# Optimization experiments

Measured on AMD Instinct MI355X. Metric: run time of the kernel, lower is better.

Reference implementation:

```python
import jax, jax.numpy as jnp
import numpy as np
import math

EMBED_DIM = 1024
NUM_HEADS = 16
HEAD_DIM = EMBED_DIM // NUM_HEADS
B, S = 4, 2048


def setup_inputs() -> dict:
    key = jax.random.key(0)
    ks = jax.random.split(key, 9)
    scale = 1.0 / math.sqrt(EMBED_DIM)
    def lin(k):
        kw, kb = jax.random.split(k)
        W = jax.random.uniform(kw, (EMBED_DIM, EMBED_DIM), jnp.float32, -scale, scale)
        b = jax.random.uniform(kb, (EMBED_DIM,), jnp.float32, -scale, scale)
        return W, b
    Wq, bq = lin(ks[0]); Wk, bk = lin(ks[1]); Wv, bv = lin(ks[2]); Wo, bo = lin(ks[3])
    x = jax.random.normal(ks[4], (B, S, EMBED_DIM), jnp.float32)
    return {"x": x, "Wq": Wq, "bq": bq, "Wk": Wk, "bk": bk,
            "Wv": Wv, "bv": bv, "Wo": Wo, "bo": bo}


def reference(x, Wq, bq, Wk, bk, Wv, bv, Wo, bo):
    Bx, Sx, E = x.shape
    def proj(W, b):
        y = jnp.einsum('bse,oe->bso', x, W) + b
        return y.reshape(Bx, Sx, NUM_HEADS, HEAD_DIM).transpose(0, 2, 1, 3)  # [B,H,S,D]
    q = proj(Wq, bq)
    k = proj(Wk, bk)
    v = proj(Wv, bv)
    scores = jnp.einsum('bhsd,bhtd->bhst', q, k) / math.sqrt(HEAD_DIM)
    # causal mask (paged_cache is None, seq_len > 1)
    causal = jnp.tril(jnp.ones((Sx, Sx), dtype=bool))
    scores = jnp.where(causal[None, None], scores, -jnp.inf)
    attn = jax.nn.softmax(scores, axis=-1)
    out = jnp.einsum('bhst,bhtd->bhsd', attn, v)
    out = out.transpose(0, 2, 1, 3).reshape(Bx, Sx, E)
    return jnp.einsum('bse,oe->bso', out, Wo) + bo
```

## Files before the change

### kernel.cpp

```cpp
#include <hip/hip_runtime.h>
#include <hip/hip_bf16.h>
#include <stdint.h>

#define EDIM 1024
#define NH   16
#define HD   64
#define BB   4
#define SS   2048
#define MROWS (BB*SS)

typedef __bf16 bf16x8 __attribute__((ext_vector_type(8)));
typedef __bf16 bf16x4 __attribute__((ext_vector_type(4)));
typedef float  f32x4  __attribute__((ext_vector_type(4)));
typedef float  f32x16 __attribute__((ext_vector_type(16)));
typedef int    int2v  __attribute__((ext_vector_type(2)));

__device__ __forceinline__ void async16(const void* g, void* lds) {
    __builtin_amdgcn_global_load_lds((__attribute__((address_space(1))) void*)(g),
                                     (__attribute__((address_space(3))) void*)(lds),
                                     16, 0, 0);
}

__device__ __forceinline__ f32x4 mfma16(bf16x8 a, bf16x8 b, f32x4 c) {
    return __builtin_amdgcn_mfma_f32_16x16x32_bf16(a, b, c, 0, 0, 0);
}
__device__ __forceinline__ f32x16 mfma32(bf16x8 a, bf16x8 b, f32x16 c) {
    return __builtin_amdgcn_mfma_f32_32x32x16_bf16(a, b, c, 0, 0, 0);
}

__device__ __forceinline__ int pkbf16(float a, float b) {
    union { __bf16 h[2]; int i; } u;
    u.h[0] = (__bf16)a; u.h[1] = (__bf16)b;
    return u.i;
}

__global__ __launch_bounds__(256) void cvt_kernel(const float* __restrict__ s,
                                                  __bf16* __restrict__ d, int n) {
    int i = (blockIdx.x * 256 + threadIdx.x) * 4;
    if (i < n) {
        float4 v = *reinterpret_cast<const float4*>(s + i);
        bf16x4 o;
        o.x = (__bf16)v.x; o.y = (__bf16)v.y; o.z = (__bf16)v.z; o.w = (__bf16)v.w;
        *reinterpret_cast<bf16x4*>(d + i) = o;
    }
}

__global__ __launch_bounds__(256) void cvt4_kernel(const float* __restrict__ s0,
                                                   const float* __restrict__ s1,
                                                   const float* __restrict__ s2,
                                                   const float* __restrict__ s3,
                                                   __bf16* __restrict__ d) {
    int m = blockIdx.x >> 10;
    const float* s = (m == 0) ? s0 : (m == 1) ? s1 : (m == 2) ? s2 : s3;
    int i = ((blockIdx.x & 1023) * 256 + threadIdx.x) * 4;
    float4 v = *reinterpret_cast<const float4*>(s + i);
    bf16x4 o;
    o.x = (__bf16)v.x; o.y = (__bf16)v.y; o.z = (__bf16)v.z; o.w = (__bf16)v.w;
    *reinterpret_cast<bf16x4*>(d + (size_t)m * (EDIM * EDIM) + i) = o;
}

struct GemmCtx {
    const __bf16 *ap0, *ap1, *bp0, *bp1;
    int wb0, wb1;
};

__device__ __forceinline__ void g_stage(GemmCtx& c, char* As, char* Bs) {
    async16(c.ap0, As + c.wb0);
    async16(c.ap1, As + c.wb1);
    async16(c.bp0, Bs + c.wb0);
    async16(c.bp1, Bs + c.wb1);
    c.ap0 += 32; c.ap1 += 32; c.bp0 += 32; c.bp1 += 32;
}

__device__ __forceinline__ void g_compute(const char* As, const char* Bs,
                                          int wm, int wn, int lrow, int lslot,
                                          f32x4 acc[4][4]) {
    bf16x8 af[4], bfr[4];
    #pragma unroll
    for (int mf = 0; mf < 4; ++mf) {
        int row = wm + mf * 16 + lrow;
        af[mf] = *reinterpret_cast<const bf16x8*>(As + row * 64 + ((lslot ^ (row & 3)) << 4));
    }
    #pragma unroll
    for (int nf = 0; nf < 4; ++nf) {
        int row = wn + nf * 16 + lrow;
        bfr[nf] = *reinterpret_cast<const bf16x8*>(Bs + row * 64 + ((lslot ^ (row & 3)) << 4));
    }
    __builtin_amdgcn_s_setprio(1);
    #pragma unroll
    for (int mf = 0; mf < 4; ++mf)
        #pragma unroll
        for (int nf = 0; nf < 4; ++nf)
            acc[mf][nf] = mfma16(af[mf], bfr[nf], acc[mf][nf]);
    __builtin_amdgcn_s_setprio(0);
}

#define GEMM_DBUF_LOOP()                                                      \
    g_stage(ctx, As0, Bs0);                                                   \
    for (int kt = 0; kt < 32; kt += 2) {                                      \
        g_stage(ctx, As1, Bs1);                                               \
        asm volatile("s_waitcnt vmcnt(4)" ::: "memory");                      \
        __builtin_amdgcn_s_barrier();                                         \
        __builtin_amdgcn_sched_barrier(0);                                    \
        g_compute(As0, Bs0, wm, wn, lrow, lslot, acc);                        \
        __builtin_amdgcn_sched_barrier(0);                                    \
        __builtin_amdgcn_s_barrier();                                         \
        if (kt + 2 < 32) {                                                    \
            g_stage(ctx, As0, Bs0);                                           \
            asm volatile("s_waitcnt vmcnt(4)" ::: "memory");                  \
        } else {                                                              \
            asm volatile("s_waitcnt vmcnt(0)" ::: "memory");                  \
        }                                                                     \
        __builtin_amdgcn_s_barrier();                                         \
        __builtin_amdgcn_sched_barrier(0);                                    \
        g_compute(As1, Bs1, wm, wn, lrow, lslot, acc);                        \
        __builtin_amdgcn_sched_barrier(0);                                    \
        __builtin_amdgcn_s_barrier();                                         \
    }

#define GEMM_PREAMBLE(Aptr, Wptr)                                             \
    const int tid = threadIdx.x;                                              \
    const int w = tid >> 6, l = tid & 63;                                     \
    const int bm = blockIdx.x * 128, bn = blockIdx.y * 128;                   \
    const int wm = (w >> 1) * 64, wn = (w & 1) * 64;                          \
    f32x4 acc[4][4] = {};                                                     \
    const int lrow = l & 15;                                                  \
    const int lslot = l >> 4;                                                 \
    const int row0 = tid >> 2, cb0 = tid & 3;                                 \
    const int row1 = 64 + row0;                                               \
    GemmCtx ctx;                                                              \
    ctx.ap0 = (Aptr) + (size_t)(bm + row0) * EDIM + ((cb0 ^ (row0 & 3)) << 3);\
    ctx.ap1 = (Aptr) + (size_t)(bm + row1) * EDIM + ((cb0 ^ (row1 & 3)) << 3);\
    ctx.bp0 = (Wptr) + (size_t)(bn + row0) * EDIM + ((cb0 ^ (row0 & 3)) << 3);\
    ctx.bp1 = (Wptr) + (size_t)(bn + row1) * EDIM + ((cb0 ^ (row1 & 3)) << 3);\
    ctx.wb0 = (w * 64) * 16;                                                  \
    ctx.wb1 = (256 + w * 64) * 16;

__global__ __launch_bounds__(256) void gemm_qkv(const __bf16* __restrict__ A,
                                                const __bf16* __restrict__ W,
                                                const float* __restrict__ bq,
                                                const float* __restrict__ bk,
                                                const float* __restrict__ bv,
                                                __bf16* __restrict__ Qb,
                                                __bf16* __restrict__ Kb,
                                                __bf16* __restrict__ Vtb) {
    __shared__ char As0[128 * 64], Bs0[128 * 64];
    __shared__ char As1[128 * 64], Bs1[128 * 64];
    GEMM_PREAMBLE(A, W)
    GEMM_DBUF_LOOP()

    const int mat = bn >> 10;
    const float* bias = (mat == 0) ? bq : (mat == 1) ? bk : bv;
    __bf16* qk = (mat == 0) ? Qb : Kb;

    #pragma unroll
    for (int nf = 0; nf < 4; ++nf) {
        int ng = bn + wn + nf * 16 + lrow;
        int nn = ng & 1023;
        int h = nn >> 6, d = nn & 63;
        float bval = bias[nn];
        #pragma unroll
        for (int mf = 0; mf < 4; ++mf) {
            #pragma unroll
            for (int r = 0; r < 4; ++r) {
                int mg = bm + wm + mf * 16 + (l >> 4) * 4 + r;
                float v = acc[mf][nf][r] + bval;
                int b = mg >> 11, s = mg & 2047;
                if (mat == 2)
                    Vtb[((size_t)(b * NH + h) * HD + d) * SS + s] = (__bf16)v;
                else
                    qk[((size_t)(b * NH + h) * SS + s) * HD + d] = (__bf16)v;
            }
        }
    }
}

__global__ __launch_bounds__(256) void gemm_out(const __bf16* __restrict__ A,
                                                const __bf16* __restrict__ W,
                                                const float* __restrict__ bias,
                                                float* __restrict__ dst) {
    __shared__ char As0[128 * 64], Bs0[128 * 64];
    __shared__ char As1[128 * 64], Bs1[128 * 64];
    GEMM_PREAMBLE(A, W)
    GEMM_DBUF_LOOP()

    #pragma unroll
    for (int nf = 0; nf < 4; ++nf) {
        int ng = bn + wn + nf * 16 + lrow;
        float bval = bias[ng];
        #pragma unroll
        for (int mf = 0; mf < 4; ++mf) {
            #pragma unroll
            for (int r = 0; r < 4; ++r) {
                int mg = bm + wm + mf * 16 + (l >> 4) * 4 + r;
                dst[(size_t)mg * EDIM + ng] = acc[mf][nf][r] + bval;
            }
        }
    }
}

#define SCL2E 0.18033688f

__global__ __launch_bounds__(512) void attn_kernel(const __bf16* __restrict__ Q,
                                                   const __bf16* __restrict__ K,
                                                   const __bf16* __restrict__ Vt,
                                                   __bf16* __restrict__ Oa,
                                                   __bf16* __restrict__ Opart,
                                                   float2* __restrict__ Ml) {
    __shared__ char ks0[64 * 128], vs0[64 * 128];
    __shared__ char ks1[64 * 128], vs1[64 * 128];

    const int bh = blockIdx.x;
    const int y = blockIdx.y;
    const bool split = (y < 8);
    const int qt = split ? (7 - (y >> 1)) : (11 - y);
    const int half = split ? (y & 1) : 0;
    const int tid = threadIdx.x;
    const int w = tid >> 6;
    const int l = tid & 63;
    const int lo = l & 31;
    const int hi = l >> 5;

    const __bf16* Qp = Q + (size_t)bh * (SS * HD);
    const __bf16* Kp = K + (size_t)bh * (SS * HD);
    const __bf16* Vp = Vt + (size_t)bh * (HD * SS);

    const int qg = qt * 256 + w * 32 + lo;
    bf16x8 qf[4];
    #pragma unroll
    for (int kc = 0; kc < 4; ++kc)
        qf[kc] = *reinterpret_cast<const bf16x8*>(Qp + (size_t)qg * HD + kc * 16 + hi * 8);

    const int nt_all = 4 * qt + 4;
    const int tcount = split ? (nt_all >> 1) : nt_all;
    const int kt0 = split ? (half * tcount) : 0;

    const int rowS = tid >> 3, cbS = tid & 7;
    const int gsS = (cbS ^ (rowS & 7)) << 3;
    const int wb = w * 1024;
    const __bf16* kp = Kp + (size_t)(kt0 * 64 + rowS) * HD + gsS;
    const __bf16* vp = Vp + (size_t)rowS * SS + kt0 * 64 + gsS;

    f32x16 oacc[2] = {};
    float mrow = -1e30f;
    float lsum = 0.f;

    const int qwhi = qt * 256 + w * 32 + 31;

    auto compute = [&](const char* ksb, const char* vsb, int kv0) {
        f32x16 acc[2] = {};
        __builtin_amdgcn_s_setprio(1);
        #pragma unroll
        for (int tb = 0; tb < 2; ++tb) {
            const int t = tb * 32 + lo;
            const char* krow = ksb + t * 128;
            const int tx = (t & 7);
            #pragma unroll
            for (int kc = 0; kc < 4; ++kc) {
                bf16x8 kf = *reinterpret_cast<const bf16x8*>(krow + ((2 * kc + hi) ^ tx) * 16);
                acc[tb] = mfma32(kf, qf[kc], acc[tb]);
            }
        }
        __builtin_amdgcn_s_setprio(0);

        if (kv0 + 63 > qg - lo) {
            #pragma unroll
            for (int tb = 0; tb < 2; ++tb)
                #pragma unroll
                for (int r = 0; r < 16; ++r) {
                    int t = kv0 + tb * 32 + ((r & 3) + 8 * (r >> 2)) + 4 * hi;
                    if (t > qg) acc[tb][r] = -1e30f;
                }
        }

        float mx = acc[0][0];
        #pragma unroll
        for (int r = 1; r < 16; ++r) mx = fmaxf(mx, acc[0][r]);
        #pragma unroll
        for (int r = 0; r < 16; ++r) mx = fmaxf(mx, acc[1][r]);
        mx = fmaxf(mx, __shfl_xor(mx, 32));
        float mxs = mx * SCL2E;
        if (!__all(mxs <= mrow + 8.0f)) {
            float mnew = fmaxf(mrow, mxs);
            float alpha = exp2f(mrow - mnew);
            mrow = mnew;
            lsum *= alpha;
            oacc[0] *= alpha;
            oacc[1] *= alpha;
        }
        float psum = 0.f;
        #pragma unroll
        for (int tb = 0; tb < 2; ++tb)
            #pragma unroll
            for (int r = 0; r < 16; ++r) {
                float p = exp2f(fmaf(acc[tb][r], SCL2E, -mrow));
                acc[tb][r] = p;
                psum += p;
            }
        lsum += psum;

        bf16x8 pa[4];
        #pragma unroll
        for (int ks2 = 0; ks2 < 4; ++ks2) {
            const int tb = ks2 >> 1, rb = (ks2 & 1) * 8;
            int a0 = pkbf16(acc[tb][rb + 0], acc[tb][rb + 1]);
            int b0 = pkbf16(acc[tb][rb + 4], acc[tb][rb + 5]);
            int a1 = pkbf16(acc[tb][rb + 2], acc[tb][rb + 3]);
            int b1 = pkbf16(acc[tb][rb + 6], acc[tb][rb + 7]);
            int2v s1 = __builtin_amdgcn_permlane32_swap(a0, b0, false, false);
            int2v s2 = __builtin_amdgcn_permlane32_swap(a1, b1, false, false);
            union { int i[4]; bf16x8 v; } u;
            u.i[0] = s1[0]; u.i[1] = s2[0]; u.i[2] = s1[1]; u.i[3] = s2[1];
            pa[ks2] = u.v;
        }

        __builtin_amdgcn_s_setprio(1);
        #pragma unroll
        for (int ks2 = 0; ks2 < 4; ++ks2) {
            #pragma unroll
            for (int db = 0; db < 2; ++db) {
                const int d = db * 32 + lo;
                bf16x8 vb = *reinterpret_cast<const bf16x8*>(
                    vsb + d * 128 + (((2 * ks2 + hi) ^ (d & 7)) * 16));
                oacc[db] = mfma32(vb, pa[ks2], oacc[db]);
            }
        }
        __builtin_amdgcn_s_setprio(0);
    };

    async16(kp, ks0 + wb);
    async16(vp, vs0 + wb);
    kp += 64 * HD; vp += 64;

    for (int kt = 0; kt < tcount; kt += 2) {
        async16(kp, ks1 + wb);
        async16(vp, vs1 + wb);
        kp += 64 * HD; vp += 64;
        asm volatile("s_waitcnt vmcnt(2)" ::: "memory");
        __builtin_amdgcn_s_barrier();
        __builtin_amdgcn_sched_barrier(0);
        if ((kt0 + kt) * 64 <= qwhi) compute(ks0, vs0, (kt0 + kt) * 64);
        __builtin_amdgcn_sched_barrier(0);
        __builtin_amdgcn_s_barrier();

        if (kt + 2 < tcount) {
            async16(kp, ks0 + wb);
            async16(vp, vs0 + wb);
            kp += 64 * HD; vp += 64;
            asm volatile("s_waitcnt vmcnt(2)" ::: "memory");
        } else {
            asm volatile("s_waitcnt vmcnt(0)" ::: "memory");
        }
        __builtin_amdgcn_s_barrier();
        __builtin_amdgcn_sched_barrier(0);
        if ((kt0 + kt + 1) * 64 <= qwhi) compute(ks1, vs1, (kt0 + kt + 1) * 64);
        __builtin_amdgcn_sched_barrier(0);
        __builtin_amdgcn_s_barrier();
    }

    float lsumt = lsum + __shfl_xor(lsum, 32);
    if (split) {
        const int qp = qg - 1024;
        __bf16* prow = Opart + (((size_t)(half * 64 + bh) * 1024) + qp) * 64;
        #pragma unroll
        for (int db = 0; db < 2; ++db) {
            #pragma unroll
            for (int g = 0; g < 4; ++g) {
                int d0 = db * 32 + g * 8 + 4 * hi;
                bf16x4 o4;
                o4.x = (__bf16)oacc[db][g * 4 + 0];
                o4.y = (__bf16)oacc[db][g * 4 + 1];
                o4.z = (__bf16)oacc[db][g * 4 + 2];
                o4.w = (__bf16)oacc[db][g * 4 + 3];
                *reinterpret_cast<bf16x4*>(prow + d0) = o4;
            }
        }
        if (hi == 0)
            Ml[(size_t)(half * 64 + bh) * 1024 + qp] = make_float2(mrow, lsumt);
    } else {
        const int b = bh >> 4, h = bh & 15;
        float inv = 1.0f / lsumt;
        __bf16* orow = Oa + ((size_t)(b * SS + qg)) * EDIM + h * HD;
        #pragma unroll
        for (int db = 0; db < 2; ++db) {
            #pragma unroll
            for (int g = 0; g < 4; ++g) {
                int d0 = db * 32 + g * 8 + 4 * hi;
                bf16x4 o4;
                o4.x = (__bf16)(oacc[db][g * 4 + 0] * inv);
                o4.y = (__bf16)(oacc[db][g * 4 + 1] * inv);
                o4.z = (__bf16)(oacc[db][g * 4 + 2] * inv);
                o4.w = (__bf16)(oacc[db][g * 4 + 3] * inv);
                *reinterpret_cast<bf16x4*>(orow + d0) = o4;
            }
        }
    }
}

__global__ __launch_bounds__(256) void merge_kernel(const __bf16* __restrict__ Opart,
                                                    const float2* __restrict__ Ml,
                                                    __bf16* __restrict__ Oa) {
    int t = blockIdx.x * 256 + threadIdx.x;
    int d8 = t & 7;
    int qp = (t >> 3) & 1023;
    int bh = t >> 13;
    size_t r0 = ((size_t)bh * 1024 + qp);
    size_t r1 = ((size_t)(64 + bh) * 1024 + qp);
    float2 ml0 = Ml[r0], ml1 = Ml[r1];
    float m = fmaxf(ml0.x, ml1.x);
    float a0 = exp2f(ml0.x - m), a1 = exp2f(ml1.x - m);
    float inv = 1.0f / (a0 * ml0.y + a1 * ml1.y);
    bf16x8 o0 = *reinterpret_cast<const bf16x8*>(Opart + r0 * 64 + d8 * 8);
    bf16x8 o1 = *reinterpret_cast<const bf16x8*>(Opart + r1 * 64 + d8 * 8);
    bf16x8 r;
    #pragma unroll
    for (int j = 0; j < 8; ++j)
        r[j] = (__bf16)((a0 * (float)o0[j] + a1 * (float)o1[j]) * inv);
    int b = bh >> 4, h = bh & 15, q = 1024 + qp;
    *reinterpret_cast<bf16x8*>(Oa + ((size_t)(b * SS + q)) * EDIM + h * HD + d8 * 8) = r;
}

extern "C" void kernel_launch(void* const* d_in, const int* in_sizes, int n_in,
                              void* d_out, int out_size, void* d_ws, size_t ws_size,
                              hipStream_t stream) {
    const float* x  = (const float*)d_in[0];
    const float* Wq = (const float*)d_in[1];
    const float* bq = (const float*)d_in[2];
    const float* Wk = (const float*)d_in[3];
    const float* bk = (const float*)d_in[4];
    const float* Wv = (const float*)d_in[5];
    const float* bv = (const float*)d_in[6];
    const float* Wo = (const float*)d_in[7];
    const float* bo = (const float*)d_in[8];

    char* ws = (char*)d_ws;
    const size_t SZ_XB  = (size_t)MROWS * EDIM * 2;
    const size_t SZ_W   = (size_t)EDIM * EDIM * 2;
    const size_t SZ_QKV = (size_t)BB * NH * SS * HD * 2;

    __bf16* xb  = (__bf16*)(ws);
    __bf16* wqb = (__bf16*)(ws + SZ_XB);
    __bf16* wob = (__bf16*)(ws + SZ_XB + 3 * SZ_W);
    __bf16* Qb  = (__bf16*)(ws + SZ_XB + 4 * SZ_W);
    __bf16* Kb  = (__bf16*)(ws + SZ_XB + 4 * SZ_W + SZ_QKV);
    __bf16* Vtb = (__bf16*)(ws + SZ_XB + 4 * SZ_W + 2 * SZ_QKV);
    __bf16* Oab = (__bf16*)(ws + SZ_XB + 4 * SZ_W + 3 * SZ_QKV);
    __bf16* Opart = (__bf16*)(ws);
    float2* Mlb   = (float2*)(ws + SZ_XB);

    cvt_kernel<<<MROWS * EDIM / 1024, 256, 0, stream>>>(x, xb, MROWS * EDIM);
    cvt4_kernel<<<4096, 256, 0, stream>>>(Wq, Wk, Wv, Wo, wqb);

    gemm_qkv<<<dim3(MROWS / 128, 3 * EDIM / 128), 256, 0, stream>>>(
        xb, wqb, bq, bk, bv, Qb, Kb, Vtb);

    attn_kernel<<<dim3(BB * NH, 12), 512, 0, stream>>>(Qb, Kb, Vtb, Oab, Opart, Mlb);
    merge_kernel<<<64 * 1024 * 8 / 256, 256, 0, stream>>>(Opart, Mlb, Oab);

    gemm_out<<<dim3(MROWS / 128, EDIM / 128), 256, 0, stream>>>(
        Oab, wob, bo, (float*)d_out);
}
```

Baseline: 201.6 us.

## Double GEMM K-tile to 64 with 8-way swizzle and vectorize V-transpose stores

The GEMM K-step per stage grows from 32 to 64 elements, so LDS buffers double to 128x128 bytes, each stage issues 8 async loads per thread, and the main loop runs half as many iterations with half as many barriers. The LDS swizzle widens from 4 to 8 slots to match the longer rows. In the QKV epilogue, the transposed V output now writes 4 consecutive sequence elements as one bf16x4 store instead of scalar stores. The cost is doubled LDS per block (64KB), which may cut occupancy.

```diff
diff --git a/kernel.cpp b/kernel.cpp
--- a/kernel.cpp
+++ b/kernel.cpp
@@ -59,55 +59,58 @@
     *reinterpret_cast<bf16x4*>(d + (size_t)m * (EDIM * EDIM) + i) = o;
 }
 
-struct GemmCtx {
-    const __bf16 *ap0, *ap1, *bp0, *bp1;
-    int wb0, wb1;
-};
-
-__device__ __forceinline__ void g_stage(GemmCtx& c, char* As, char* Bs) {
-    async16(c.ap0, As + c.wb0);
-    async16(c.ap1, As + c.wb1);
-    async16(c.bp0, Bs + c.wb0);
-    async16(c.bp1, Bs + c.wb1);
-    c.ap0 += 32; c.ap1 += 32; c.bp0 += 32; c.bp1 += 32;
+struct GCtx { const __bf16 *ap, *bp; };
+
+__device__ __forceinline__ void g_stage(GCtx& c, char* As, char* Bs, int wb) {
+    #pragma unroll
+    for (int i = 0; i < 4; ++i) {
+        async16(c.ap + i * 32 * EDIM, As + wb + i * 4096);
+        async16(c.bp + i * 32 * EDIM, Bs + wb + i * 4096);
+    }
+    c.ap += 64; c.bp += 64;
 }
 
 __device__ __forceinline__ void g_compute(const char* As, const char* Bs,
                                           int wm, int wn, int lrow, int lslot,
                                           f32x4 acc[4][4]) {
-    bf16x8 af[4], bfr[4];
     #pragma unroll
-    for (int mf = 0; mf < 4; ++mf) {
-        int row = wm + mf * 16 + lrow;
-        af[mf] = *reinterpret_cast<const bf16x8*>(As + row * 64 + ((lslot ^ (row & 3)) << 4));
-    }
-    #pragma unroll
-    for (int nf = 0; nf < 4; ++nf) {
-        int row = wn + nf * 16 + lrow;
-        bfr[nf] = *reinterpret_cast<const bf16x8*>(Bs + row * 64 + ((lslot ^ (row & 3)) << 4));
-    }
-    __builtin_amdgcn_s_setprio(1);
-    #pragma unroll
-    for (int mf = 0; mf < 4; ++mf)
-        #pragma unroll
-        for (int nf = 0; nf < 4; ++nf)
-            acc[mf][nf] = mfma16(af[mf], bfr[nf], acc[mf][nf]);
-    __builtin_amdgcn_s_setprio(0);
+    for (int kc = 0; kc < 2; ++kc) {
+        bf16x8 af[4], bfr[4];
+        #pragma unroll
+        for (int mf = 0; mf < 4; ++mf) {
+            int row = wm + mf * 16 + lrow;
+            af[mf] = *reinterpret_cast<const bf16x8*>(
+                As + row * 128 + (((kc * 4 + lslot) ^ (row & 7)) << 4));
+        }
+        #pragma unroll
+        for (int nf = 0; nf < 4; ++nf) {
+            int row = wn + nf * 16 + lrow;
+            bfr[nf] = *reinterpret_cast<const bf16x8*>(
+                Bs + row * 128 + (((kc * 4 + lslot) ^ (row & 7)) << 4));
+        }
+        __builtin_amdgcn_s_setprio(1);
+        #pragma unroll
+        for (int mf = 0; mf < 4; ++mf)
+            #pragma unroll
+            for (int nf = 0; nf < 4; ++nf)
+                acc[mf][nf] = mfma16(af[mf], bfr[nf], acc[mf][nf]);
+        __builtin_amdgcn_s_setprio(0);
+    }
 }
 
 #define GEMM_DBUF_LOOP()                                                      \
-    g_stage(ctx, As0, Bs0);                                                   \
-    for (int kt = 0; kt < 32; kt += 2) {                                      \
-        g_stage(ctx, As1, Bs1);                                               \
-        asm volatile("s_waitcnt vmcnt(4)" ::: "memory");                      \
+    g_stage(ctx, As0, Bs0, wb);                                               \
+    for (int kt = 0; kt < 16; kt += 2) {                                      \
+        g_stage(ctx, As1, Bs1, wb);                                           \
+        asm volatile("s_waitcnt vmcnt(8)" ::: "memory");                      \
         __builtin_amdgcn_s_barrier();                                         \
         __builtin_amdgcn_sched_barrier(0);                                    \
         g_compute(As0, Bs0, wm, wn, lrow, lslot, acc);                        \
         __builtin_amdgcn_sched_barrier(0);                                    \
         __builtin_amdgcn_s_barrier();                                         \
-        if (kt + 2 < 32) {                                                    \
-            g_stage(ctx, As0, Bs0);                                           \
-            asm volatile("s_waitcnt vmcnt(4)" ::: "memory");                  \
+        if (kt + 2 < 16) {                                                    \
+            g_stage(ctx, As0, Bs0, wb);                                       \
+            asm volatile("s_waitcnt vmcnt(8)" ::: "memory");                  \
         } else {                                                              \
             asm volatile("s_waitcnt vmcnt(0)" ::: "memory");                  \
         }                                                                     \
@@ -126,15 +129,12 @@
     f32x4 acc[4][4] = {};                                                     \
     const int lrow = l & 15;                                                  \
     const int lslot = l >> 4;                                                 \
-    const int row0 = tid >> 2, cb0 = tid & 3;                                 \
-    const int row1 = 64 + row0;                                               \
-    GemmCtx ctx;                                                              \
-    ctx.ap0 = (Aptr) + (size_t)(bm + row0) * EDIM + ((cb0 ^ (row0 & 3)) << 3);\
-    ctx.ap1 = (Aptr) + (size_t)(bm + row1) * EDIM + ((cb0 ^ (row1 & 3)) << 3);\
-    ctx.bp0 = (Wptr) + (size_t)(bn + row0) * EDIM + ((cb0 ^ (row0 & 3)) << 3);\
-    ctx.bp1 = (Wptr) + (size_t)(bn + row1) * EDIM + ((cb0 ^ (row1 & 3)) << 3);\
-    ctx.wb0 = (w * 64) * 16;                                                  \
-    ctx.wb1 = (256 + w * 64) * 16;
+    const int row0 = tid >> 3;                                                \
+    const int gs = ((tid & 7) ^ (row0 & 7)) << 3;                             \
+    const int wb = w * 1024;                                                  \
+    GCtx ctx;                                                                 \
+    ctx.ap = (Aptr) + (size_t)(bm + row0) * EDIM + gs;                        \
+    ctx.bp = (Wptr) + (size_t)(bn + row0) * EDIM + gs;
 
 __global__ __launch_bounds__(256) void gemm_qkv(const __bf16* __restrict__ A,
                                                 const __bf16* __restrict__ W,
@@ -144,32 +144,49 @@
                                                 __bf16* __restrict__ Qb,
                                                 __bf16* __restrict__ Kb,
                                                 __bf16* __restrict__ Vtb) {
-    __shared__ char As0[128 * 64], Bs0[128 * 64];
-    __shared__ char As1[128 * 64], Bs1[128 * 64];
+    __shared__ char As0[128 * 128], Bs0[128 * 128];
+    __shared__ char As1[128 * 128], Bs1[128 * 128];
     GEMM_PREAMBLE(A, W)
     GEMM_DBUF_LOOP()
 
     const int mat = bn >> 10;
     const float* bias = (mat == 0) ? bq : (mat == 1) ? bk : bv;
-    __bf16* qk = (mat == 0) ? Qb : Kb;
-
-    #pragma unroll
-    for (int nf = 0; nf < 4; ++nf) {
-        int ng = bn + wn + nf * 16 + lrow;
-        int nn = ng & 1023;
-        int h = nn >> 6, d = nn & 63;
-        float bval = bias[nn];
-        #pragma unroll
-        for (int mf = 0; mf < 4; ++mf) {
-            #pragma unroll
-            for (int r = 0; r < 4; ++r) {
-                int mg = bm + wm + mf * 16 + (l >> 4) * 4 + r;
-                float v = acc[mf][nf][r] + bval;
-                int b = mg >> 11, s = mg & 2047;
-                if (mat == 2)
-                    Vtb[((size_t)(b * NH + h) * HD + d) * SS + s] = (__bf16)v;
-                else
-                    qk[((size_t)(b * NH + h) * SS + s) * HD + d] = (__bf16)v;
+
+    if (mat == 2) {
+        #pragma unroll
+        for (int nf = 0; nf < 4; ++nf) {
+            int nn = (bn + wn + nf * 16 + lrow) & 1023;
+            int h = nn >> 6, d = nn & 63;
+            float bval = bias[nn];
+            #pragma unroll
+            for (int mf = 0; mf < 4; ++mf) {
+                int mg0 = bm + wm + mf * 16 + (l >> 4) * 4;
+                int b = mg0 >> 11, s = mg0 & 2047;
+                bf16x4 o4;
+                o4.x = (__bf16)(acc[mf][nf][0] + bval);
+                o4.y = (__bf16)(acc[mf][nf][1] + bval);
+                o4.z = (__bf16)(acc[mf][nf][2] + bval);
+                o4.w = (__bf16)(acc[mf][nf][3] + bval);
+                *reinterpret_cast<bf16x4*>(
+                    Vtb + ((size_t)(b * NH + h) * HD + d) * SS + s) = o4;
+            }
+        }
+    } else {
+        __bf16* qk = (mat == 0) ? Qb : Kb;
+        #pragma unroll
+        for (int nf = 0; nf < 4; ++nf) {
+            int nn = (bn + wn + nf * 16 + lrow) & 1023;
+            int h = nn >> 6, d = nn & 63;
+            float bval = bias[nn];
+            #pragma unroll
+            for (int mf = 0; mf < 4; ++mf) {
+                #pragma unroll
+                for (int r = 0; r < 4; ++r) {
+                    int mg = bm + wm + mf * 16 + (l >> 4) * 4 + r;
+                    int b = mg >> 11, s = mg & 2047;
+                    qk[((size_t)(b * NH + h) * SS + s) * HD + d] =
+                        (__bf16)(acc[mf][nf][r] + bval);
+                }
             }
         }
     }
@@ -179,8 +196,8 @@
                                                 const __bf16* __restrict__ W,
                                                 const float* __restrict__ bias,
                                                 float* __restrict__ dst) {
-    __shared__ char As0[128 * 64], Bs0[128 * 64];
-    __shared__ char As1[128 * 64], Bs1[128 * 64];
+    __shared__ char As0[128 * 128], Bs0[128 * 128];
+    __shared__ char As1[128 * 128], Bs1[128 * 128];
     GEMM_PREAMBLE(A, W)
     GEMM_DBUF_LOOP()
 
```

New measurement: 175.8 us, median of 2. -12.8%, faster.
